# Kernel optimization log

Hardware: AMD Instinct MI355X
Metric: run time of the kernel (lower is better)

Reference implementation:

```python
import jax, jax.numpy as jnp
import numpy as np

HEADS, DH = 8, 64  # SelfAttention defaults: heads=8, dim_head=64


def _layernorm(x, g, b, eps=1e-5):
    mu = x.mean(-1, keepdims=True)
    var = ((x - mu) ** 2).mean(-1, keepdims=True)
    return (x - mu) / jnp.sqrt(var + eps) * g + b


def setup_inputs() -> dict:
    key = jax.random.key(0)
    ks = jax.random.split(key, 13)
    B, H, W, D, P = 1, 256, 256, 64, 128
    inner = HEADS * DH
    s = 0.05  # weight scale to keep logits in a sane range
    return {
        "x": jax.random.normal(ks[0], (B, H, W, D), jnp.float32),
        "pair_bias": jax.random.normal(ks[1], (B, W, W, P), jnp.float32),
        "Wq_w": jax.random.normal(ks[2], (D, inner), jnp.float32) * s,
        "Wkv_w": jax.random.normal(ks[3], (D, 2 * inner), jnp.float32) * s,
        "Wout_w": jax.random.normal(ks[4], (inner, D), jnp.float32) * s,
        "bout_w": jnp.zeros((D,), jnp.float32),
        "Wq_h": jax.random.normal(ks[5], (D, inner), jnp.float32) * s,
        "Wkv_h": jax.random.normal(ks[6], (D, 2 * inner), jnp.float32) * s,
        "Wout_h": jax.random.normal(ks[7], (inner, D), jnp.float32) * s,
        "bout_h": jnp.zeros((D,), jnp.float32),
        "pair_ln_g": jnp.ones((P,), jnp.float32),
        "pair_ln_b": jnp.zeros((P,), jnp.float32),
        "W_pair": jax.random.normal(ks[8], (P, HEADS), jnp.float32) * s,
    }


def _qkv(x2d, Wq, Wkv):
    # x2d: (N, L, D) -> q, k, v each (N, heads, L, dh)
    N, L, _ = x2d.shape
    q = (x2d @ Wq).reshape(N, L, HEADS, DH).transpose(0, 2, 1, 3)
    kv = (x2d @ Wkv).reshape(N, L, 2, HEADS, DH)
    k = kv[:, :, 0].transpose(0, 2, 1, 3)
    v = kv[:, :, 1].transpose(0, 2, 1, 3)
    return q, k, v


def reference(x, pair_bias, Wq_w, Wkv_w, Wout_w, bout_w,
              Wq_h, Wkv_h, Wout_h, bout_h, pair_ln_g, pair_ln_b, W_pair):
    B, H, W, D = x.shape  # B=1, H=n_seqs, W=length, D=dim
    scale = DH ** -0.5

    # ---- width attention: attend over seq dim H, batched per column (b*w) ----
    xw = jnp.transpose(x, (0, 2, 1, 3)).reshape(B * W, H, D)
    q, k, v = _qkv(xw, Wq_w, Wkv_w)
    dots = jnp.einsum('bhid,bhjd->bhij', q, k) * scale  # (B*W, heads, H, H)
    attn = jax.nn.softmax(dots, axis=-1)
    ow = jnp.einsum('bhij,bhjd->bhid', attn, v)
    ow = ow.transpose(0, 2, 1, 3).reshape(B * W, H, HEADS * DH)
    ow = ow @ Wout_w + bout_w
    w_out = ow.reshape(B, W, H, D).transpose(0, 2, 1, 3)  # (B, H, W, D)

    # ---- height attention: tied over seq dim (tie_attn_dim=H), pair bias ----
    xh = x.reshape(B * H, W, D)
    q, k, v = _qkv(xh, Wq_h, Wkv_h)           # (B*H, heads, W, dh)
    q = q.reshape(B, H, HEADS, W, DH)
    k = k.reshape(B, H, HEADS, W, DH)
    v = v.reshape(B, H, HEADS, W, DH)
    dots = jnp.einsum('brhid,brhjd->bhij', q, k) * scale * (H ** -0.5)  # (B, heads, W, W)
    pb = _layernorm(pair_bias, pair_ln_g, pair_ln_b) @ W_pair  # (B, W, W, heads)
    dots = dots + pb.transpose(0, 3, 1, 2)
    attn = jax.nn.softmax(dots, axis=-1)
    oh = jnp.einsum('bhij,brhjd->brhid', attn, v)  # (B, H, heads, W, dh)
    oh = oh.transpose(0, 1, 3, 2, 4).reshape(B, H, W, HEADS * DH)
    h_out = oh @ Wout_h + bout_h  # (B, H, W, D)

    return (w_out + h_out) * 0.5
```

## Files before the change

### kernel.cpp

```cpp
#include <hip/hip_runtime.h>
#include <hip/hip_bf16.h>

typedef __hip_bfloat16 bf16;
typedef __attribute__((ext_vector_type(8))) short bf16x8;
typedef __attribute__((ext_vector_type(4))) float f32x4;

#define MFMA16(a, b, c) __builtin_amdgcn_mfma_f32_16x16x32_bf16(a, b, c, 0, 0, 0)

#define HH 256
#define WW 256
#define NHEADS 8
#define NROWS 65536


__device__ __forceinline__ bf16x8 cvt8(const float* f) {
  bf16x8 r;
  bf16* h = (bf16*)&r;
#pragma unroll
  for (int i = 0; i < 8; i++) h[i] = __float2bfloat16(f[i]);
  return r;
}

__global__ void __launch_bounds__(256) k_xT2(const float* __restrict__ x,
                                             bf16* __restrict__ xh,
                                             bf16* __restrict__ xw) {
  const size_t idx = ((size_t)blockIdx.x * 256 + threadIdx.x) * 4;
  const float4 v = *(const float4*)(x + idx);
  bf16 tmp[4];
  tmp[0] = __float2bfloat16(v.x);
  tmp[1] = __float2bfloat16(v.y);
  tmp[2] = __float2bfloat16(v.z);
  tmp[3] = __float2bfloat16(v.w);
  *(uint2*)(xh + idx) = *(const uint2*)tmp;
  const int n = (int)(idx >> 6), d = (int)(idx & 63);
  const int h = n >> 8, w = n & 255;
  *(uint2*)(xw + (((size_t)((w << 8) | h)) << 6) + d) = *(const uint2*)tmp;
}

__global__ void __launch_bounds__(256) k_wt2(const float* __restrict__ Wq_w,
                                             const float* __restrict__ Wkv_w,
                                             const float* __restrict__ Wq_h,
                                             const float* __restrict__ Wkv_h,
                                             bf16* __restrict__ Wt_w,
                                             bf16* __restrict__ Wt_h) {
  int idx = blockIdx.x * 256 + threadIdx.x;
  const float* Wq = Wq_w;
  const float* Wkv = Wkv_w;
  bf16* Wt = Wt_w;
  if (idx >= 98304) { idx -= 98304; Wq = Wq_h; Wkv = Wkv_h; Wt = Wt_h; }
  const int k = idx / 1536, c = idx - k * 1536;
  const float val = (c < 512) ? Wq[k * 512 + c] : Wkv[k * 1024 + (c - 512)];
  Wt[(size_t)c * 64 + k] = __float2bfloat16(val);
}

__global__ void __launch_bounds__(256) k_wo(const float* __restrict__ Wout_w,
                                            const float* __restrict__ Wout_h,
                                            bf16* __restrict__ Wo_w,
                                            bf16* __restrict__ Wo_h) {
  int idx = blockIdx.x * 256 + threadIdx.x;
  const float* W = Wout_w;
  bf16* dst = Wo_w;
  if (idx >= 32768) { idx -= 32768; W = Wout_h; dst = Wo_h; }
  const int c = idx >> 9, d = idx & 511;
  dst[idx] = __float2bfloat16(W[d * 64 + c]);
}

__global__ void __launch_bounds__(256, 2)
k_width_fused(const bf16* __restrict__ xw, const bf16* __restrict__ Wt,
              bf16* __restrict__ Ow) {
  __shared__ __align__(16) char smem[65536];
  bf16* Qs = (bf16*)smem;
  bf16* Ks = (bf16*)(smem + 32768);
  bf16* Vt = (bf16*)(smem + 49152);
  const int w = blockIdx.x, head = blockIdx.y;
  const int tid = threadIdx.x, lane = tid & 63, wv = tid >> 6;
  bf16* Ps = (bf16*)(smem + wv * 5120);
  const int m16 = lane & 15, kq = lane >> 4;
  const int i0 = wv * 64;
  const bf16* xcol = xw + (size_t)w * 256 * 64;

  bf16x8 af[4][2];
#pragma unroll
  for (int mt = 0; mt < 4; mt++) {
    const bf16* xr = xcol + (size_t)(i0 + mt * 16 + m16) * 64 + kq * 8;
    af[mt][0] = *(const bf16x8*)xr;
    af[mt][1] = *(const bf16x8*)(xr + 32);
  }
#pragma unroll
  for (int nt = 0; nt < 4; nt++) {
    const bf16* wp = Wt + (size_t)(head * 64 + nt * 16 + m16) * 64 + kq * 8;
    const bf16x8 w0 = *(const bf16x8*)wp;
    const bf16x8 w1 = *(const bf16x8*)(wp + 32);
#pragma unroll
    for (int mt = 0; mt < 4; mt++) {
      f32x4 a = (f32x4){0.f, 0.f, 0.f, 0.f};
      a = MFMA16(af[mt][0], w0, a);
      a = MFMA16(af[mt][1], w1, a);
#pragma unroll
      for (int r = 0; r < 4; r++) {
        const int i = i0 + mt * 16 + kq * 4 + r;
        const int d = nt * 16 + m16;
        Qs[i * 64 + (((d >> 3) ^ (i & 7)) << 3) + (d & 7)] = __float2bfloat16(a[r]);
      }
    }
  }
  __syncthreads();
  bf16x8 qf[4][2];
#pragma unroll
  for (int it = 0; it < 4; it++)
#pragma unroll
    for (int ks = 0; ks < 2; ks++)
      qf[it][ks] = *(const bf16x8*)&Qs[(i0 + it * 16 + m16) * 64 +
                                       (((ks * 4 + kq) ^ (m16 & 7)) << 3)];

  f32x4 acc[4][4];
#pragma unroll
  for (int a = 0; a < 4; a++)
#pragma unroll
    for (int b = 0; b < 4; b++) acc[a][b] = (f32x4){0.f, 0.f, 0.f, 0.f};
  float rsum[4][4];
#pragma unroll
  for (int a = 0; a < 4; a++)
#pragma unroll
    for (int r = 0; r < 4; r++) rsum[a][r] = 0.f;

#pragma unroll 1
  for (int half = 0; half < 2; half++) {
    if (half) __syncthreads();
    bf16x8 afk[2][2];
#pragma unroll
    for (int mt = 0; mt < 2; mt++) {
      const int jrow = half * 128 + wv * 32 + mt * 16 + m16;
      const bf16* xr = xcol + (size_t)jrow * 64 + kq * 8;
      afk[mt][0] = *(const bf16x8*)xr;
      afk[mt][1] = *(const bf16x8*)(xr + 32);
    }
#pragma unroll
    for (int nt = 0; nt < 4; nt++) {
      const int d = nt * 16 + m16;
      {
        const bf16* wp = Wt + (size_t)(512 + head * 64 + d) * 64 + kq * 8;
        const bf16x8 w0 = *(const bf16x8*)wp;
        const bf16x8 w1 = *(const bf16x8*)(wp + 32);
#pragma unroll
        for (int mt = 0; mt < 2; mt++) {
          f32x4 a = (f32x4){0.f, 0.f, 0.f, 0.f};
          a = MFMA16(afk[mt][0], w0, a);
          a = MFMA16(afk[mt][1], w1, a);
#pragma unroll
          for (int r = 0; r < 4; r++) {
            const int jl = wv * 32 + mt * 16 + kq * 4 + r;
            Ks[jl * 64 + (((d >> 3) ^ (jl & 7)) << 3) + (d & 7)] = __float2bfloat16(a[r]);
          }
        }
      }
      {
        const bf16* wp = Wt + (size_t)(1024 + head * 64 + d) * 64 + kq * 8;
        const bf16x8 w0 = *(const bf16x8*)wp;
        const bf16x8 w1 = *(const bf16x8*)(wp + 32);
#pragma unroll
        for (int mt = 0; mt < 2; mt++) {
          f32x4 a = (f32x4){0.f, 0.f, 0.f, 0.f};
          a = MFMA16(afk[mt][0], w0, a);
          a = MFMA16(afk[mt][1], w1, a);
          const int jb = wv * 32 + mt * 16 + kq * 4;
          bf16 tmp[4];
#pragma unroll
          for (int r = 0; r < 4; r++) tmp[r] = __float2bfloat16(a[r]);
          *(uint2*)&Vt[d * 128 + (((jb >> 3) ^ (d & 7)) << 3) + (jb & 7)] =
              *(const uint2*)tmp;
        }
      }
    }
    __syncthreads();
#pragma unroll 1
    for (int jcl = 0; jcl < 4; jcl++) {
      bf16x8 kf[2][2];
#pragma unroll
      for (int jt = 0; jt < 2; jt++) {
        const int j = jcl * 32 + jt * 16 + m16;
#pragma unroll
        for (int ks = 0; ks < 2; ks++)
          kf[jt][ks] = *(const bf16x8*)&Ks[j * 64 + (((ks * 4 + kq) ^ (j & 7)) << 3)];
      }
#pragma unroll
      for (int it = 0; it < 4; it++)
#pragma unroll
        for (int jt = 0; jt < 2; jt++) {
          f32x4 s = (f32x4){0.f, 0.f, 0.f, 0.f};
          s = MFMA16(qf[it][0], kf[jt][0], s);
          s = MFMA16(qf[it][1], kf[jt][1], s);
#pragma unroll
          for (int r = 0; r < 4; r++) {
            float p = __expf(s[r] * 0.125f);
            rsum[it][r] += p;
            Ps[(it * 16 + kq * 4 + r) * 40 + jt * 16 + m16] = __float2bfloat16(p);
          }
        }
      bf16x8 pf[4], vf[4];
#pragma unroll
      for (int it = 0; it < 4; it++)
        pf[it] = *(const bf16x8*)&Ps[(it * 16 + m16) * 40 + kq * 8];
#pragma unroll
      for (int dt = 0; dt < 4; dt++)
        vf[dt] = *(const bf16x8*)&Vt[(dt * 16 + m16) * 128 +
                                     (((jcl * 4 + kq) ^ (m16 & 7)) << 3)];
#pragma unroll
      for (int it = 0; it < 4; it++)
#pragma unroll
        for (int dt = 0; dt < 4; dt++) acc[it][dt] = MFMA16(pf[it], vf[dt], acc[it][dt]);
    }
  }

#pragma unroll
  for (int it = 0; it < 4; it++)
#pragma unroll
    for (int r = 0; r < 4; r++) {
      float s = rsum[it][r];
      s += __shfl_xor(s, 1); s += __shfl_xor(s, 2);
      s += __shfl_xor(s, 4); s += __shfl_xor(s, 8);
      rsum[it][r] = 1.f / s;
    }
#pragma unroll
  for (int it = 0; it < 4; it++)
#pragma unroll
    for (int dt = 0; dt < 4; dt++)
#pragma unroll
      for (int r = 0; r < 4; r++) {
        const int i = i0 + it * 16 + kq * 4 + r;
        Ow[((size_t)(w * 256 + i)) * 512 + head * 64 + dt * 16 + m16] =
            __float2bfloat16(acc[it][dt][r] * rsum[it][r]);
      }
}

__global__ void __launch_bounds__(256, 2)
k_dots_f(const bf16* __restrict__ xh, const bf16* __restrict__ Wt, float* __restrict__ dp) {
  __shared__ __align__(16) bf16 Qs[64 * 72];
  __shared__ __align__(16) bf16 Ks[64 * 72];
  const int tile = blockIdx.x, head = blockIdx.y, rc = blockIdx.z;
  const int i0 = (tile >> 2) * 64, j0 = (tile & 3) * 64;
  const int tid = threadIdx.x, lane = tid & 63, wv = tid >> 6;
  const int m16 = lane & 15, kq = lane >> 4;
  float* slice = dp + (size_t)rc * 524288 + (size_t)head * 65536;

  const bf16* WtQ = Wt + (size_t)(head * 64) * 64 + kq * 8;
  const bf16* WtK = Wt + (size_t)(512 + head * 64) * 64 + kq * 8;

  f32x4 acc[4];
#pragma unroll
  for (int b = 0; b < 4; b++) acc[b] = (f32x4){0.f, 0.f, 0.f, 0.f};

  const int lrow = wv * 16 + kq * 4;

#pragma unroll 1
  for (int rr = 0; rr < 32; rr++) {
    const int rbase = (rc * 32 + rr) * 256;
    __syncthreads();
    {
      const bf16* xr = xh + (size_t)(rbase + i0 + wv * 16 + m16) * 64 + kq * 8;
      const bf16x8 qa0 = *(const bf16x8*)xr;
      const bf16x8 qa1 = *(const bf16x8*)(xr + 32);
      const bf16* yr = xh + (size_t)(rbase + j0 + wv * 16 + m16) * 64 + kq * 8;
      const bf16x8 ka0 = *(const bf16x8*)yr;
      const bf16x8 ka1 = *(const bf16x8*)(yr + 32);
#pragma unroll
      for (int nt = 0; nt < 4; nt++) {
        const bf16* wq = WtQ + (size_t)(nt * 16 + m16) * 64;
        f32x4 aq = (f32x4){0.f, 0.f, 0.f, 0.f};
        aq = MFMA16(qa0, *(const bf16x8*)wq, aq);
        aq = MFMA16(qa1, *(const bf16x8*)(wq + 32), aq);
        const bf16* wk = WtK + (size_t)(nt * 16 + m16) * 64;
        f32x4 ak = (f32x4){0.f, 0.f, 0.f, 0.f};
        ak = MFMA16(ka0, *(const bf16x8*)wk, ak);
        ak = MFMA16(ka1, *(const bf16x8*)(wk + 32), ak);
#pragma unroll
        for (int r = 0; r < 4; r++) {
          Qs[(lrow + r) * 72 + nt * 16 + m16] = __float2bfloat16(aq[r]);
          Ks[(lrow + r) * 72 + nt * 16 + m16] = __float2bfloat16(ak[r]);
        }
      }
    }
    __syncthreads();
#pragma unroll
    for (int ks = 0; ks < 2; ks++) {
      bf16x8 af = *(const bf16x8*)&Qs[(wv * 16 + m16) * 72 + ks * 32 + kq * 8];
      bf16x8 bfr[4];
#pragma unroll
      for (int jt = 0; jt < 4; jt++)
        bfr[jt] = *(const bf16x8*)&Ks[(jt * 16 + m16) * 72 + ks * 32 + kq * 8];
#pragma unroll
      for (int jt = 0; jt < 4; jt++) acc[jt] = MFMA16(af, bfr[jt], acc[jt]);
    }
  }
  const float sc = 1.f / 128.f;
#pragma unroll
  for (int jt = 0; jt < 4; jt++)
#pragma unroll
    for (int r = 0; r < 4; r++)
      slice[(size_t)(i0 + wv * 16 + kq * 4 + r) * 256 + j0 + jt * 16 + m16] = acc[jt][r] * sc;
}

__global__ void __launch_bounds__(256) k_pb(const float* __restrict__ pb,
                                            const float* __restrict__ g,
                                            const float* __restrict__ bb,
                                            const float* __restrict__ Wp,
                                            float* __restrict__ dots) {
  __shared__ float sn[4][128];
  const int tid = threadIdx.x, lane = tid & 63, wv = tid >> 6;
  const size_t ij = (size_t)blockIdx.x * 4 + wv;
  const float2 xv = *(const float2*)(pb + ij * 128 + lane * 2);

  float s = xv.x + xv.y;
#pragma unroll
  for (int o = 1; o < 64; o <<= 1) s += __shfl_xor(s, o);
  const float mu = s * (1.f / 128.f);
  const float d0 = xv.x - mu, d1 = xv.y - mu;
  float s2 = d0 * d0 + d1 * d1;
#pragma unroll
  for (int o = 1; o < 64; o <<= 1) s2 += __shfl_xor(s2, o);
  const float inv = rsqrtf(s2 * (1.f / 128.f) + 1e-5f);

  sn[wv][lane * 2 + 0] = d0 * inv * g[lane * 2 + 0] + bb[lane * 2 + 0];
  sn[wv][lane * 2 + 1] = d1 * inv * g[lane * 2 + 1] + bb[lane * 2 + 1];

  const int h = lane & 7, gp = lane >> 3;
  float a = 0.f;
#pragma unroll
  for (int p0 = 0; p0 < 16; p0++) {
    const int p = gp * 16 + p0;
    a += sn[wv][p] * Wp[p * 8 + h];
  }
  a += __shfl_xor(a, 8);
  a += __shfl_xor(a, 16);
  a += __shfl_xor(a, 32);
  if (lane < 8) dots[(size_t)h * 65536 + ij] += a;
}

__global__ void __launch_bounds__(256) k_softmax8(const float* __restrict__ dp,
                                                  bf16* __restrict__ P) {
  __shared__ float red[4];
  const int i = blockIdx.x, head = blockIdx.y, t = threadIdx.x;
  const size_t base = (size_t)head * 65536 + i * 256 + t;
  float lg = 0.f;
#pragma unroll
  for (int s = 0; s < 8; s++) lg += dp[(size_t)s * 524288 + base];
  const float e = __expf(lg);
  float s = e;
#pragma unroll
  for (int o = 1; o < 64; o <<= 1) s += __shfl_xor(s, o);
  if ((t & 63) == 0) red[t >> 6] = s;
  __syncthreads();
  const float S = red[0] + red[1] + red[2] + red[3];
  P[base] = __float2bfloat16(e / S);
}

__global__ void __launch_bounds__(256, 2)
k_h_pv_f(const bf16* __restrict__ P, const bf16* __restrict__ xh,
         const bf16* __restrict__ Wt, bf16* __restrict__ Oh) {
  __shared__ __align__(16) bf16 Vt[64 * 256];
  const int r = blockIdx.x, head = blockIdx.y;
  const int tid = threadIdx.x, lane = tid & 63, wv = tid >> 6;
  const int m16 = lane & 15, kq = lane >> 4;

  {
    const bf16* WtV = Wt + (size_t)(1024 + head * 64) * 64 + kq * 8;
#pragma unroll
    for (int mt = 0; mt < 4; mt++) {
      const int jb16 = wv * 64 + mt * 16;
      const bf16* xr = xh + (size_t)(r * 256 + jb16 + m16) * 64 + kq * 8;
      const bf16x8 a0 = *(const bf16x8*)xr;
      const bf16x8 a1 = *(const bf16x8*)(xr + 32);
#pragma unroll
      for (int nt = 0; nt < 4; nt++) {
        const int d = nt * 16 + m16;
        const bf16* wp = WtV + (size_t)(nt * 16 + m16) * 64;
        f32x4 a = (f32x4){0.f, 0.f, 0.f, 0.f};
        a = MFMA16(a0, *(const bf16x8*)wp, a);
        a = MFMA16(a1, *(const bf16x8*)(wp + 32), a);
        const int j = jb16 + kq * 4;
        bf16 tmp[4];
#pragma unroll
        for (int r2 = 0; r2 < 4; r2++) tmp[r2] = __float2bfloat16(a[r2]);
        *(uint2*)&Vt[d * 256 + (((j >> 3) ^ (d & 7)) << 3) + (j & 7)] = *(const uint2*)tmp;
      }
    }
  }

  const bf16* Pb = P + (size_t)head * 65536;
  const int i0 = wv * 64;
  auto loadP = [&](int ks, bf16x8 pf[4]) {
#pragma unroll
    for (int it = 0; it < 4; it++)
      pf[it] = *(const bf16x8*)(Pb + (size_t)(i0 + it * 16 + m16) * 256 + ks * 32 + kq * 8);
  };
  bf16x8 pcur[4];
  loadP(0, pcur);
  __syncthreads();

  f32x4 acc[4][4];
#pragma unroll
  for (int a = 0; a < 4; a++)
#pragma unroll
    for (int b = 0; b < 4; b++) acc[a][b] = (f32x4){0.f, 0.f, 0.f, 0.f};

#pragma unroll 1
  for (int ks = 0; ks < 8; ks++) {
    bf16x8 pnext[4];
    if (ks < 7) loadP(ks + 1, pnext);
    bf16x8 vf[4];
#pragma unroll
    for (int dt = 0; dt < 4; dt++)
      vf[dt] = *(const bf16x8*)&Vt[(dt * 16 + m16) * 256 + (((ks * 4 + kq) ^ (m16 & 7)) << 3)];
#pragma unroll
    for (int it = 0; it < 4; it++)
#pragma unroll
      for (int dt = 0; dt < 4; dt++) acc[it][dt] = MFMA16(pcur[it], vf[dt], acc[it][dt]);
    if (ks < 7) {
#pragma unroll
      for (int it = 0; it < 4; it++) pcur[it] = pnext[it];
    }
  }
#pragma unroll
  for (int it = 0; it < 4; it++)
#pragma unroll
    for (int dt = 0; dt < 4; dt++)
#pragma unroll
      for (int r2 = 0; r2 < 4; r2++) {
        const int i = i0 + it * 16 + kq * 4 + r2;
        Oh[((size_t)(r * 256 + i)) * 512 + head * 64 + dt * 16 + m16] =
            __float2bfloat16(acc[it][dt][r2]);
      }
}

__global__ void __launch_bounds__(256) k_outproj(const bf16* __restrict__ Ow,
                                                 const bf16* __restrict__ Oh,
                                                 const bf16* __restrict__ Wow,
                                                 const bf16* __restrict__ Woh,
                                                 const float* __restrict__ bw,
                                                 const float* __restrict__ bh,
                                                 float* __restrict__ out) {
  const int tid = threadIdx.x, lane = tid & 63, wv = tid >> 6;
  const int m16 = lane & 15, kq = lane >> 4;
  const int nA = blockIdx.x * 64 + wv * 16 + m16;
  const int wA = ((nA & 255) << 8) | (nA >> 8);

  const bf16* aw = Ow + (size_t)wA * 512 + kq * 8;
  const bf16* ah = Oh + (size_t)nA * 512 + kq * 8;

  f32x4 acc[4];
#pragma unroll
  for (int ct = 0; ct < 4; ct++) acc[ct] = (f32x4){0.f, 0.f, 0.f, 0.f};

#pragma unroll 1
  for (int kc = 0; kc < 16; kc++) {
    const bf16x8 afw = *(const bf16x8*)(aw + kc * 32);
    const bf16x8 afh = *(const bf16x8*)(ah + kc * 32);
#pragma unroll
    for (int ct = 0; ct < 4; ct++) {
      const bf16x8 bfw = *(const bf16x8*)(Wow + (size_t)(ct * 16 + m16) * 512 + kc * 32 + kq * 8);
      const bf16x8 bfh = *(const bf16x8*)(Woh + (size_t)(ct * 16 + m16) * 512 + kc * 32 + kq * 8);
      acc[ct] = MFMA16(afw, bfw, acc[ct]);
      acc[ct] = MFMA16(afh, bfh, acc[ct]);
    }
  }
  const int n0 = blockIdx.x * 64 + wv * 16 + kq * 4;
#pragma unroll
  for (int ct = 0; ct < 4; ct++) {
    const int c = ct * 16 + m16;
    const float bias = 0.5f * (bw[c] + bh[c]);
#pragma unroll
    for (int r = 0; r < 4; r++)
      out[(size_t)(n0 + r) * 64 + c] = 0.5f * acc[ct][r] + bias;
  }
}

extern "C" void kernel_launch(void* const* d_in, const int* in_sizes, int n_in,
                              void* d_out, int out_size, void* d_ws, size_t ws_size,
                              hipStream_t stream) {
  const float* x      = (const float*)d_in[0];
  const float* pair   = (const float*)d_in[1];
  const float* Wq_w   = (const float*)d_in[2];
  const float* Wkv_w  = (const float*)d_in[3];
  const float* Wout_w = (const float*)d_in[4];
  const float* bout_w = (const float*)d_in[5];
  const float* Wq_h   = (const float*)d_in[6];
  const float* Wkv_h  = (const float*)d_in[7];
  const float* Wout_h = (const float*)d_in[8];
  const float* bout_h = (const float*)d_in[9];
  const float* ln_g   = (const float*)d_in[10];
  const float* ln_b   = (const float*)d_in[11];
  const float* W_pair = (const float*)d_in[12];
  float* out = (float*)d_out;

  char* ws = (char*)d_ws;
  bf16* R0 = (bf16*)ws;
  bf16* xh = (bf16*)(ws + 67108864);
  bf16* xw = (bf16*)(ws + 67108864 + 8388608);
  bf16* R2 = (bf16*)(ws + 134217728);
  bf16* Wt_w = (bf16*)(ws + 201326592);
  bf16* Wt_h = (bf16*)(ws + 201326592 + 393216);
  bf16* P  = (bf16*)(ws + 201326592 + 786432);
  bf16* Wo_w = (bf16*)(ws + 201326592 + 1835008);
  bf16* Wo_h = Wo_w + 32768;
  float* dp = out;

  k_xT2<<<4096, 256, 0, stream>>>(x, xh, xw);
  k_wt2<<<768, 256, 0, stream>>>(Wq_w, Wkv_w, Wq_h, Wkv_h, Wt_w, Wt_h);
  k_wo<<<256, 256, 0, stream>>>(Wout_w, Wout_h, Wo_w, Wo_h);

  k_width_fused<<<dim3(WW, NHEADS), 256, 0, stream>>>(xw, Wt_w, R0);

  k_dots_f<<<dim3(16, NHEADS, 8), 256, 0, stream>>>(xh, Wt_h, dp);
  k_pb<<<65536 / 4, 256, 0, stream>>>(pair, ln_g, ln_b, W_pair, dp);
  k_softmax8<<<dim3(256, NHEADS), 256, 0, stream>>>(dp, P);
  k_h_pv_f<<<dim3(HH, NHEADS), 256, 0, stream>>>(P, xh, Wt_h, R2);

  k_outproj<<<1024, 256, 0, stream>>>(R0, R2, Wo_w, Wo_h, bout_w, bout_h, out);
}
```

Measured before the change: 445.7 us.

## Split width-attention block across 8 waves with 32 query rows each

```diff
diff --git a/kernel.cpp b/kernel.cpp
--- a/kernel.cpp
+++ b/kernel.cpp
@@ -65,7 +65,7 @@
   dst[idx] = __float2bfloat16(W[d * 64 + c]);
 }
 
-__global__ void __launch_bounds__(256, 2)
+__global__ void __launch_bounds__(512, 1)
 k_width_fused(const bf16* __restrict__ xw, const bf16* __restrict__ Wt,
               bf16* __restrict__ Ow) {
   __shared__ __align__(16) char smem[65536];
@@ -74,14 +74,14 @@
   bf16* Vt = (bf16*)(smem + 49152);
   const int w = blockIdx.x, head = blockIdx.y;
   const int tid = threadIdx.x, lane = tid & 63, wv = tid >> 6;
-  bf16* Ps = (bf16*)(smem + wv * 5120);
+  bf16* Ps = (bf16*)(smem + wv * 2560);
   const int m16 = lane & 15, kq = lane >> 4;
-  const int i0 = wv * 64;
+  const int i0 = wv * 32;
   const bf16* xcol = xw + (size_t)w * 256 * 64;
 
-  bf16x8 af[4][2];
-#pragma unroll
-  for (int mt = 0; mt < 4; mt++) {
+  bf16x8 af[2][2];
+#pragma unroll
+  for (int mt = 0; mt < 2; mt++) {
     const bf16* xr = xcol + (size_t)(i0 + mt * 16 + m16) * 64 + kq * 8;
     af[mt][0] = *(const bf16x8*)xr;
     af[mt][1] = *(const bf16x8*)(xr + 32);
@@ -92,7 +92,7 @@
     const bf16x8 w0 = *(const bf16x8*)wp;
     const bf16x8 w1 = *(const bf16x8*)(wp + 32);
 #pragma unroll
-    for (int mt = 0; mt < 4; mt++) {
+    for (int mt = 0; mt < 2; mt++) {
       f32x4 a = (f32x4){0.f, 0.f, 0.f, 0.f};
       a = MFMA16(af[mt][0], w0, a);
       a = MFMA16(af[mt][1], w1, a);
@@ -105,65 +105,53 @@
     }
   }
   __syncthreads();
-  bf16x8 qf[4][2];
-#pragma unroll
-  for (int it = 0; it < 4; it++)
+  bf16x8 qf[2][2];
+#pragma unroll
+  for (int it = 0; it < 2; it++)
 #pragma unroll
     for (int ks = 0; ks < 2; ks++)
       qf[it][ks] = *(const bf16x8*)&Qs[(i0 + it * 16 + m16) * 64 +
                                        (((ks * 4 + kq) ^ (m16 & 7)) << 3)];
 
-  f32x4 acc[4][4];
-#pragma unroll
-  for (int a = 0; a < 4; a++)
+  f32x4 acc[2][4];
+#pragma unroll
+  for (int a = 0; a < 2; a++)
 #pragma unroll
     for (int b = 0; b < 4; b++) acc[a][b] = (f32x4){0.f, 0.f, 0.f, 0.f};
-  float rsum[4][4];
-#pragma unroll
-  for (int a = 0; a < 4; a++)
+  float rsum[2][4];
+#pragma unroll
+  for (int a = 0; a < 2; a++)
 #pragma unroll
     for (int r = 0; r < 4; r++) rsum[a][r] = 0.f;
 
 #pragma unroll 1
   for (int half = 0; half < 2; half++) {
     if (half) __syncthreads();
-    bf16x8 afk[2][2];
-#pragma unroll
-    for (int mt = 0; mt < 2; mt++) {
-      const int jrow = half * 128 + wv * 32 + mt * 16 + m16;
+    {
+      const int jrow = half * 128 + wv * 16 + m16;
       const bf16* xr = xcol + (size_t)jrow * 64 + kq * 8;
-      afk[mt][0] = *(const bf16x8*)xr;
-      afk[mt][1] = *(const bf16x8*)(xr + 32);
-    }
-#pragma unroll
-    for (int nt = 0; nt < 4; nt++) {
-      const int d = nt * 16 + m16;
-      {
-        const bf16* wp = Wt + (size_t)(512 + head * 64 + d) * 64 + kq * 8;
-        const bf16x8 w0 = *(const bf16x8*)wp;
-        const bf16x8 w1 = *(const bf16x8*)(wp + 32);
-#pragma unroll
-        for (int mt = 0; mt < 2; mt++) {
+      const bf16x8 ak0 = *(const bf16x8*)xr;
+      const bf16x8 ak1 = *(const bf16x8*)(xr + 32);
+#pragma unroll
+      for (int nt = 0; nt < 4; nt++) {
+        const int d = nt * 16 + m16;
+        {
+          const bf16* wp = Wt + (size_t)(512 + head * 64 + d) * 64 + kq * 8;
           f32x4 a = (f32x4){0.f, 0.f, 0.f, 0.f};
-          a = MFMA16(afk[mt][0], w0, a);
-          a = MFMA16(afk[mt][1], w1, a);
+          a = MFMA16(ak0, *(const bf16x8*)wp, a);
+          a = MFMA16(ak1, *(const bf16x8*)(wp + 32), a);
 #pragma unroll
           for (int r = 0; r < 4; r++) {
-            const int jl = wv * 32 + mt * 16 + kq * 4 + r;
+            const int jl = wv * 16 + kq * 4 + r;
             Ks[jl * 64 + (((d >> 3) ^ (jl & 7)) << 3) + (d & 7)] = __float2bfloat16(a[r]);
           }
         }
-      }
-      {
-        const bf16* wp = Wt + (size_t)(1024 + head * 64 + d) * 64 + kq * 8;
-        const bf16x8 w0 = *(const bf16x8*)wp;
-        const bf16x8 w1 = *(const bf16x8*)(wp + 32);
-#pragma unroll
-        for (int mt = 0; mt < 2; mt++) {
+        {
+          const bf16* wp = Wt + (size_t)(1024 + head * 64 + d) * 64 + kq * 8;
           f32x4 a = (f32x4){0.f, 0.f, 0.f, 0.f};
-          a = MFMA16(afk[mt][0], w0, a);
-          a = MFMA16(afk[mt][1], w1, a);
-          const int jb = wv * 32 + mt * 16 + kq * 4;
+          a = MFMA16(ak0, *(const bf16x8*)wp, a);
+          a = MFMA16(ak1, *(const bf16x8*)(wp + 32), a);
+          const int jb = wv * 16 + kq * 4;
           bf16 tmp[4];
 #pragma unroll
           for (int r = 0; r < 4; r++) tmp[r] = __float2bfloat16(a[r]);
@@ -184,7 +172,7 @@
           kf[jt][ks] = *(const bf16x8*)&Ks[j * 64 + (((ks * 4 + kq) ^ (j & 7)) << 3)];
       }
 #pragma unroll
-      for (int it = 0; it < 4; it++)
+      for (int it = 0; it < 2; it++)
 #pragma unroll
         for (int jt = 0; jt < 2; jt++) {
           f32x4 s = (f32x4){0.f, 0.f, 0.f, 0.f};
@@ -197,23 +185,23 @@
             Ps[(it * 16 + kq * 4 + r) * 40 + jt * 16 + m16] = __float2bfloat16(p);
           }
         }
-      bf16x8 pf[4], vf[4];
-#pragma unroll
-      for (int it = 0; it < 4; it++)
+      bf16x8 pf[2], vf[4];
+#pragma unroll
+      for (int it = 0; it < 2; it++)
         pf[it] = *(const bf16x8*)&Ps[(it * 16 + m16) * 40 + kq * 8];
 #pragma unroll
       for (int dt = 0; dt < 4; dt++)
         vf[dt] = *(const bf16x8*)&Vt[(dt * 16 + m16) * 128 +
                                      (((jcl * 4 + kq) ^ (m16 & 7)) << 3)];
 #pragma unroll
-      for (int it = 0; it < 4; it++)
+      for (int it = 0; it < 2; it++)
 #pragma unroll
         for (int dt = 0; dt < 4; dt++) acc[it][dt] = MFMA16(pf[it], vf[dt], acc[it][dt]);
     }
   }
 
 #pragma unroll
-  for (int it = 0; it < 4; it++)
+  for (int it = 0; it < 2; it++)
 #pragma unroll
     for (int r = 0; r < 4; r++) {
       float s = rsum[it][r];
@@ -222,7 +210,7 @@
       rsum[it][r] = 1.f / s;
     }
 #pragma unroll
-  for (int it = 0; it < 4; it++)
+  for (int it = 0; it < 2; it++)
 #pragma unroll
     for (int dt = 0; dt < 4; dt++)
 #pragma unroll
@@ -508,7 +496,7 @@
   k_wt2<<<768, 256, 0, stream>>>(Wq_w, Wkv_w, Wq_h, Wkv_h, Wt_w, Wt_h);
   k_wo<<<256, 256, 0, stream>>>(Wout_w, Wout_h, Wo_w, Wo_h);
 
-  k_width_fused<<<dim3(WW, NHEADS), 256, 0, stream>>>(xw, Wt_w, R0);
+  k_width_fused<<<dim3(WW, NHEADS), 512, 0, stream>>>(xw, Wt_w, R0);
 
   k_dots_f<<<dim3(16, NHEADS, 8), 256, 0, stream>>>(xh, Wt_h, dp);
   k_pb<<<65536 / 4, 256, 0, stream>>>(pair, ln_g, ln_b, W_pair, dp);
```

Result: slower. 474.3 us (+6.4%).
